# Kernel optimization log

Measured on AMD Instinct MI355X. Metric: run time of the kernel, lower is better.

## Reference

```python
import jax, jax.numpy as jnp
import numpy as np
from itertools import combinations

H_RANK_MAX = 2
TP_RANK_MAX = 2
BASIS_RANK_MAX = 2
DIM = 3
N_NODES = 50000
N_EDGES = 400000
N_CHANNELS = 16
R_CUT = 10.0  # radial cutoff for Bessel RBF (assumed)


def find_combinations(a_max, b_max, s):
    if s > a_max + b_max or s < 0:
        return []
    return [(a, s - a) for a in range(max(0, s - b_max), min(a_max, s) + 1)]


def contraction_is_valid(n_in, n_out):
    # legs are removed in pairs (Kronecker-delta contractions)
    return (n_in >= n_out) and ((n_in - n_out) % 2 == 0)


def _matchings(legs):
    # all perfect matchings of an even-size list of leg indices
    if not legs:
        yield []
        return
    a = legs[0]
    for i in range(1, len(legs)):
        rest = legs[1:i] + legs[i + 1:]
        for m in _matchings(rest):
            yield [(a, legs[i])] + m


def contraction_specs(a, b, c_out):
    # all einsum strings contracting an [E,K,dim^a] x [E,K,dim^b] tensor product
    # (a+b legs total) down to c_out free Cartesian legs, pairing the rest.
    n = a + b
    specs = []
    for free in combinations(range(n), c_out):
        paired = [i for i in range(n) if i not in free]
        for m in _matchings(paired):
            lbl = {}
            it = iter('mnopqrstuvwxyz')
            for f in free:
                lbl[f] = next(it)
            for (i, j) in m:
                L = next(it)
                lbl[i] = L
                lbl[j] = L
            sa = ''.join(lbl[i] for i in range(a))
            sb = ''.join(lbl[i] for i in range(a, n))
            so = ''.join(lbl[f] for f in free)
            specs.append(f'ek{sa},ek{sb}->ek{so}')
    return specs


def e_rbf(r, n):
    # Bessel radial basis: n is [K,1], r is [E] -> [K,E]
    return jnp.sqrt(2.0 / R_CUT) * jnp.sin(n * jnp.pi * r / R_CUT) / r


def tensor_prod(r, order):
    # repeated outer product of unit vectors: order 0 -> [E], order k -> [E] + [DIM]*k
    out = jnp.ones(r.shape[0], dtype=r.dtype)
    for _ in range(order):
        out = jnp.einsum('e...,ed->e...d', out, r)
    return out


def setup_inputs() -> dict:
    key = jax.random.key(0)
    ks = jax.random.split(key, 7)
    h0 = jax.random.normal(ks[0], (N_NODES, N_CHANNELS), jnp.float32)
    h1 = jax.random.normal(ks[1], (N_NODES, N_CHANNELS, DIM), jnp.float32)
    h2 = jax.random.normal(ks[2], (N_NODES, N_CHANNELS, DIM, DIM), jnp.float32)
    pos = jax.random.normal(ks[3], (N_NODES, DIM), jnp.float32)
    channel_weights = jax.random.normal(ks[4], (H_RANK_MAX + 1, N_CHANNELS, N_CHANNELS), jnp.float32)
    src = jax.random.randint(ks[5], (N_EDGES,), 0, N_NODES, dtype=jnp.int32)
    off = jax.random.randint(ks[6], (N_EDGES,), 1, N_NODES, dtype=jnp.int32)
    dst = (src + off) % N_NODES  # no self-loops -> no zero distances
    edge_index = jnp.stack([src, dst])
    return {"h0": h0, "h1": h1, "h2": h2, "pos": pos,
            "channel_weights": channel_weights, "edge_index": edge_index}


def reference(h0, h1, h2, pos, channel_weights, edge_index):
    h = [h0, h1, h2]
    src, dst = edge_index[0], edge_index[1]
    rel = pos[src] - pos[dst]                       # [E,3]
    dists = jnp.linalg.norm(rel, axis=-1)           # [E]
    unit = rel / dists[:, None]
    hg = [g[dst] for g in h]                        # per-edge gathered features
    # NOTE: the original forward computes channel-mixed self.h with channel_weights
    # but the contraction loop uses the UNMIXED gathered h (h[split[0]]); replicated here,
    # so channel_weights does not affect the output (zero gradient).
    n_vals = jnp.arange(1, N_CHANNELS + 1, dtype=dists.dtype)[:, None]  # [K,1]
    radial = e_rbf(dists, n_vals).reshape(N_EDGES, N_CHANNELS)  # faithful reshape (not transpose), as in source
    r_raw = [tensor_prod(unit, o) for o in range(TP_RANK_MAX + 1)]
    r_w = [jnp.einsum('ek,e...->ek...', radial, t) for t in r_raw]  # [E,K]+[3]*b
    outs = [None] * (BASIS_RANK_MAX + 1)
    for n_ind in range(H_RANK_MAX + TP_RANK_MAX + 1):
        for (a, b) in find_combinations(H_RANK_MAX, TP_RANK_MAX, n_ind):
            for br in range(BASIS_RANK_MAX + 1):
                if contraction_is_valid(n_ind, br):
                    for spec in contraction_specs(a, b, br):
                        t = jnp.einsum(spec, hg[a], r_w[b])
                        outs[br] = t if outs[br] is None else outs[br] + t
    # sum over paths (done incrementally above == stack + 'i...->...'), scatter to nodes
    res = []
    for t in outs:
        if t is not None:
            res.append(jax.ops.segment_sum(t, src, num_segments=N_NODES))
    return tuple(res)
```

## Files before the change

kernel.cpp:

```cpp
#include <hip/hip_runtime.h>
#include <math.h>

#define N_NODES   50000
#define N_EDGES   400000
#define NCH       16
#define CAP       48
#define NSTRIPE   8
#define TPB       256
#define NBN       ((N_NODES + TPB - 1) / TPB)
#define NB_EDGES  ((N_EDGES + TPB - 1) / TPB)


__global__ void build_kernel(const float* __restrict__ pos,
                             const int* __restrict__ src,
                             const int* __restrict__ dst,
                             float* __restrict__ dists,
                             int* __restrict__ cnt,
                             float4* __restrict__ edata,
                             int* __restrict__ eArr) {
    int e = blockIdx.x * TPB + threadIdx.x;
    if (e >= N_EDGES) return;
    int s = src[e];
    int d = dst[e];
    float rx = pos[3 * s + 0] - pos[3 * d + 0];
    float ry = pos[3 * s + 1] - pos[3 * d + 1];
    float rz = pos[3 * s + 2] - pos[3 * d + 2];
    float dist = sqrtf(rx * rx + ry * ry + rz * rz);
    dists[e] = dist;
    float inv = 1.0f / dist;
    int slot = atomicAdd(&cnt[s], 1);
    if (slot < CAP) {
        int idx = s * CAP + slot;
        float4 ed;
        ed.x = rx * inv;
        ed.y = ry * inv;
        ed.z = rz * inv;
        ed.w = __int_as_float(d);
        edata[idx] = ed;
        eArr[idx] = e;
    }
}

__global__ void node_wave_fast(const float* __restrict__ h0,
                               const float* __restrict__ h1,
                               const float* __restrict__ h2,
                               const int* __restrict__ cnt,
                               const float4* __restrict__ edata,
                               const int* __restrict__ eArr,
                               const float* __restrict__ dists,
                               float* __restrict__ out0,
                               float* __restrict__ out1,
                               float* __restrict__ out2) {
    int gid = blockIdx.x * TPB + threadIdx.x;
    int node = gid >> 6;
    if (node >= N_NODES) return;
    int lane = threadIdx.x & 63;
    int k = lane & 15;
    int j = lane >> 4;
    int m = cnt[node];
    if (m > CAP) m = CAP;
    int base = node * CAP;

    float acc0 = 0.0f;
    float acc1[3] = {0.0f, 0.0f, 0.0f};
    float acc2[9] = {0.0f, 0.0f, 0.0f, 0.0f, 0.0f, 0.0f, 0.0f, 0.0f, 0.0f};

    int c = j;
    float4 ed;
    int e = 0;
    if (c < m) { ed = edata[base + c]; e = eArr[base + c]; }
    while (c < m) {
        int cn = c + 4;
        float4 edn = ed;
        int en = e;
        if (cn < m) { edn = edata[base + cn]; en = eArr[base + cn]; }

        int d = __float_as_int(ed.w);

        unsigned f = (unsigned)e * NCH + (unsigned)k;
        unsigned n_idx = f / (unsigned)N_EDGES;
        unsigned e_idx = f - n_idx * (unsigned)N_EDGES;
        float r = dists[e_idx];
        float R = 0.44721359549995794f *
                  __sinf((float)(n_idx + 1) * 0.3141592653589793f * r) / r;

        float ux = ed.x, uy = ed.y, uz = ed.z;
        float u[3] = {ux, uy, uz};

        float A0 = h0[d * NCH + k];
        const float* a1p = h1 + ((size_t)d * NCH + k) * 3;
        float A1[3] = {a1p[0], a1p[1], a1p[2]};
        const float* a2p = h2 + ((size_t)d * NCH + k) * 9;
        float A2[9];
#pragma unroll
        for (int q2 = 0; q2 < 9; ++q2) A2[q2] = a2p[q2];

        float d1 = A1[0] * ux + A1[1] * uy + A1[2] * uz;
        float tA = A2[0] + A2[4] + A2[8];
        float v0 = A2[0] * ux + A2[1] * uy + A2[2] * uz;
        float v1 = A2[3] * ux + A2[4] * uy + A2[5] * uz;
        float v2 = A2[6] * ux + A2[7] * uy + A2[8] * uz;
        float w0 = A2[0] * ux + A2[3] * uy + A2[6] * uz;
        float w1 = A2[1] * ux + A2[4] * uy + A2[7] * uz;
        float w2 = A2[2] * ux + A2[5] * uy + A2[8] * uz;
        float q = ux * v0 + uy * v1 + uz * v2;

        acc0 += R * (2.0f * A0 + d1 + 2.0f * tA + 2.0f * q);

        float svw[3] = {v0 + w0, v1 + w1, v2 + w2};
        float a0t = A0 + tA;
#pragma unroll
        for (int mm = 0; mm < 3; ++mm) {
            acc1[mm] += R * (A0 * u[mm] + 2.0f * A1[mm] + 2.0f * d1 * u[mm]
                             + svw[mm] + tA * u[mm]);
#pragma unroll
            for (int nn = 0; nn < 3; ++nn) {
                acc2[3 * mm + nn] += R * (a0t * u[mm] * u[nn] + A1[mm] * u[nn]
                                          + 2.0f * A2[3 * mm + nn]
                                          + 2.0f * svw[mm] * u[nn]);
            }
        }

        ed = edn;
        e = en;
        c = cn;
    }

    acc0 += __shfl_xor(acc0, 16, 64);
    acc0 += __shfl_xor(acc0, 32, 64);
#pragma unroll
    for (int mm = 0; mm < 3; ++mm) {
        acc1[mm] += __shfl_xor(acc1[mm], 16, 64);
        acc1[mm] += __shfl_xor(acc1[mm], 32, 64);
    }
#pragma unroll
    for (int mm = 0; mm < 9; ++mm) {
        acc2[mm] += __shfl_xor(acc2[mm], 16, 64);
        acc2[mm] += __shfl_xor(acc2[mm], 32, 64);
    }

    if (j == 0) {
        int t = node * NCH + k;
        out0[t] = acc0;
        float* o1p = out1 + (size_t)t * 3;
#pragma unroll
        for (int mm = 0; mm < 3; ++mm) o1p[mm] = acc1[mm];
        float* o2p = out2 + (size_t)t * 9;
#pragma unroll
        for (int mm = 0; mm < 9; ++mm) o2p[mm] = acc2[mm];
    }
}


__global__ void fb_geom_hist(const float* __restrict__ pos,
                             const int* __restrict__ src,
                             const int* __restrict__ dst,
                             float* __restrict__ dists,
                             int* __restrict__ cnt8,
                             int* __restrict__ rankArr) {
    int e = blockIdx.x * TPB + threadIdx.x;
    if (e >= N_EDGES) return;
    int stripe = blockIdx.x & (NSTRIPE - 1);
    int s = src[e];
    int d = dst[e];
    float rx = pos[3 * s + 0] - pos[3 * d + 0];
    float ry = pos[3 * s + 1] - pos[3 * d + 1];
    float rz = pos[3 * s + 2] - pos[3 * d + 2];
    dists[e] = sqrtf(rx * rx + ry * ry + rz * rz);
    rankArr[e] = atomicAdd(&cnt8[stripe * N_NODES + s], 1);
}

__global__ void fb_scan(const int* __restrict__ cnt8,
                        int* __restrict__ incl,
                        int* __restrict__ bsum) {
    __shared__ int sh[TPB];
    int tid = threadIdx.x;
    int i = blockIdx.x * TPB + tid;
    int tot = 0;
    if (i < N_NODES) {
#pragma unroll
        for (int c = 0; c < NSTRIPE; ++c) tot += cnt8[c * N_NODES + i];
    }
    sh[tid] = tot;
    __syncthreads();
    for (int s = 1; s < TPB; s <<= 1) {
        int x = 0;
        if (tid >= s) x = sh[tid - s];
        __syncthreads();
        if (tid >= s) sh[tid] += x;
        __syncthreads();
    }
    if (i < N_NODES) incl[i] = sh[tid];
    if (tid == TPB - 1) bsum[blockIdx.x] = sh[TPB - 1];
}

__global__ void fb_final(const int* __restrict__ cnt8,
                         const int* __restrict__ incl,
                         const int* __restrict__ bsum,
                         int* __restrict__ offsets,
                         int* __restrict__ copyBase) {
    __shared__ int sh[TPB];
    int tid = threadIdx.x;
    int b = blockIdx.x;
    sh[tid] = (tid < b) ? bsum[tid] : 0;
    __syncthreads();
    for (int s = 128; s > 0; s >>= 1) {
        if (tid < s) sh[tid] += sh[tid + s];
        __syncthreads();
    }
    int base = sh[0];
    int i = b * TPB + tid;
    if (i < N_NODES) {
        int cv[NSTRIPE];
        int tot = 0;
#pragma unroll
        for (int c = 0; c < NSTRIPE; ++c) { cv[c] = cnt8[c * N_NODES + i]; tot += cv[c]; }
        int off = base + incl[i] - tot;
        offsets[i] = off;
        int run = off;
#pragma unroll
        for (int c = 0; c < NSTRIPE; ++c) { copyBase[c * N_NODES + i] = run; run += cv[c]; }
    }
    if (b == 0 && tid == 0) offsets[N_NODES] = N_EDGES;
}

__global__ void fb_fill(const int* __restrict__ src,
                        const int* __restrict__ dst,
                        const float* __restrict__ pos,
                        const float* __restrict__ dists,
                        const int* __restrict__ copyBase,
                        const int* __restrict__ rankArr,
                        float4* __restrict__ edata,
                        int* __restrict__ csr) {
    int e = blockIdx.x * TPB + threadIdx.x;
    if (e >= N_EDGES) return;
    int stripe = blockIdx.x & (NSTRIPE - 1);
    int s = src[e];
    int d = dst[e];
    float rx = pos[3 * s + 0] - pos[3 * d + 0];
    float ry = pos[3 * s + 1] - pos[3 * d + 1];
    float rz = pos[3 * s + 2] - pos[3 * d + 2];
    float inv = 1.0f / dists[e];
    int slot = copyBase[stripe * N_NODES + s] + rankArr[e];
    float4 ed;
    ed.x = rx * inv;
    ed.y = ry * inv;
    ed.z = rz * inv;
    ed.w = __int_as_float(d);
    edata[slot] = ed;
    csr[slot] = e;
}

__global__ void fb_main(const float* __restrict__ h0,
                        const float* __restrict__ h1,
                        const float* __restrict__ h2,
                        const int* __restrict__ offsets,
                        const float4* __restrict__ edata,
                        const int* __restrict__ csr,
                        const float* __restrict__ dists,
                        float* __restrict__ out0,
                        float* __restrict__ out1,
                        float* __restrict__ out2) {
    int gid = blockIdx.x * TPB + threadIdx.x;
    int node = gid >> 6;
    if (node >= N_NODES) return;
    int lane = threadIdx.x & 63;
    int k = lane & 15;
    int j = lane >> 4;
    int beg = offsets[node];
    int end = offsets[node + 1];

    float acc0 = 0.0f;
    float acc1[3] = {0.0f, 0.0f, 0.0f};
    float acc2[9] = {0.0f, 0.0f, 0.0f, 0.0f, 0.0f, 0.0f, 0.0f, 0.0f, 0.0f};

    int i = beg + j;
    float4 ed;
    int e = 0;
    if (i < end) { ed = edata[i]; e = csr[i]; }
    while (i < end) {
        int inext = i + 4;
        float4 edn = ed;
        int en = e;
        if (inext < end) { edn = edata[inext]; en = csr[inext]; }

        int d = __float_as_int(ed.w);
        unsigned f = (unsigned)e * NCH + (unsigned)k;
        unsigned n_idx = f / (unsigned)N_EDGES;
        unsigned e_idx = f - n_idx * (unsigned)N_EDGES;
        float r = dists[e_idx];
        float R = 0.44721359549995794f *
                  __sinf((float)(n_idx + 1) * 0.3141592653589793f * r) / r;

        float ux = ed.x, uy = ed.y, uz = ed.z;
        float u[3] = {ux, uy, uz};

        float A0 = h0[d * NCH + k];
        const float* a1p = h1 + ((size_t)d * NCH + k) * 3;
        float A1[3] = {a1p[0], a1p[1], a1p[2]};
        const float* a2p = h2 + ((size_t)d * NCH + k) * 9;
        float A2[9];
#pragma unroll
        for (int q2 = 0; q2 < 9; ++q2) A2[q2] = a2p[q2];

        float d1 = A1[0] * ux + A1[1] * uy + A1[2] * uz;
        float tA = A2[0] + A2[4] + A2[8];
        float v0 = A2[0] * ux + A2[1] * uy + A2[2] * uz;
        float v1 = A2[3] * ux + A2[4] * uy + A2[5] * uz;
        float v2 = A2[6] * ux + A2[7] * uy + A2[8] * uz;
        float w0 = A2[0] * ux + A2[3] * uy + A2[6] * uz;
        float w1 = A2[1] * ux + A2[4] * uy + A2[7] * uz;
        float w2 = A2[2] * ux + A2[5] * uy + A2[8] * uz;
        float q = ux * v0 + uy * v1 + uz * v2;

        acc0 += R * (2.0f * A0 + d1 + 2.0f * tA + 2.0f * q);

        float svw[3] = {v0 + w0, v1 + w1, v2 + w2};
        float a0t = A0 + tA;
#pragma unroll
        for (int mm = 0; mm < 3; ++mm) {
            acc1[mm] += R * (A0 * u[mm] + 2.0f * A1[mm] + 2.0f * d1 * u[mm]
                             + svw[mm] + tA * u[mm]);
#pragma unroll
            for (int nn = 0; nn < 3; ++nn) {
                acc2[3 * mm + nn] += R * (a0t * u[mm] * u[nn] + A1[mm] * u[nn]
                                          + 2.0f * A2[3 * mm + nn]
                                          + 2.0f * svw[mm] * u[nn]);
            }
        }

        ed = edn;
        e = en;
        i = inext;
    }

    acc0 += __shfl_xor(acc0, 16, 64);
    acc0 += __shfl_xor(acc0, 32, 64);
#pragma unroll
    for (int mm = 0; mm < 3; ++mm) {
        acc1[mm] += __shfl_xor(acc1[mm], 16, 64);
        acc1[mm] += __shfl_xor(acc1[mm], 32, 64);
    }
#pragma unroll
    for (int mm = 0; mm < 9; ++mm) {
        acc2[mm] += __shfl_xor(acc2[mm], 16, 64);
        acc2[mm] += __shfl_xor(acc2[mm], 32, 64);
    }

    if (j == 0) {
        int t = node * NCH + k;
        out0[t] = acc0;
        float* o1p = out1 + (size_t)t * 3;
#pragma unroll
        for (int mm = 0; mm < 3; ++mm) o1p[mm] = acc1[mm];
        float* o2p = out2 + (size_t)t * 9;
#pragma unroll
        for (int mm = 0; mm < 9; ++mm) o2p[mm] = acc2[mm];
    }
}


extern "C" void kernel_launch(void* const* d_in, const int* in_sizes, int n_in,
                              void* d_out, int out_size, void* d_ws, size_t ws_size,
                              hipStream_t stream) {
    const float* h0  = (const float*)d_in[0];
    const float* h1  = (const float*)d_in[1];
    const float* h2  = (const float*)d_in[2];
    const float* pos = (const float*)d_in[3];
    const int* edge_index = (const int*)d_in[5];
    const int* src = edge_index;
    const int* dst = edge_index + N_EDGES;

    float* out = (float*)d_out;
    float* out0 = out;
    float* out1 = out + (size_t)N_NODES * NCH;
    float* out2 = out + (size_t)N_NODES * NCH * 4;

    size_t need = (size_t)N_NODES * CAP * 16 + (size_t)N_NODES * CAP * 4
                + (size_t)N_EDGES * 4 + (size_t)N_NODES * 4;

    if (ws_size >= need) {
        float4* edata = (float4*)d_ws;
        int* eArr     = (int*)(edata + (size_t)N_NODES * CAP);
        float* dists  = (float*)(eArr + (size_t)N_NODES * CAP);
        int* cnt      = (int*)(dists + N_EDGES);

        hipMemsetAsync(cnt, 0, N_NODES * sizeof(int), stream);
        build_kernel<<<NB_EDGES, TPB, 0, stream>>>(pos, src, dst, dists, cnt, edata, eArr);
        node_wave_fast<<<(N_NODES * 64 + TPB - 1) / TPB, TPB, 0, stream>>>(
            h0, h1, h2, cnt, edata, eArr, dists, out0, out1, out2);
    } else {
        float4* edata   = (float4*)d_ws;
        float*  dists   = (float*)(edata + N_EDGES);
        int* cnt8       = (int*)(dists + N_EDGES);
        int* rankArr    = cnt8 + NSTRIPE * N_NODES;
        int* incl       = rankArr + N_EDGES;
        int* bsum       = incl + N_NODES;
        int* offsets    = bsum + 256;
        int* copyBase   = offsets + N_NODES + 1;
        int* csr        = copyBase + NSTRIPE * N_NODES;

        hipMemsetAsync(cnt8, 0, NSTRIPE * N_NODES * sizeof(int), stream);
        fb_geom_hist<<<NB_EDGES, TPB, 0, stream>>>(pos, src, dst, dists, cnt8, rankArr);
        fb_scan<<<NBN, TPB, 0, stream>>>(cnt8, incl, bsum);
        fb_final<<<NBN, TPB, 0, stream>>>(cnt8, incl, bsum, offsets, copyBase);
        fb_fill<<<NB_EDGES, TPB, 0, stream>>>(src, dst, pos, dists, copyBase, rankArr, edata, csr);
        fb_main<<<(N_NODES * 64 + TPB - 1) / TPB, TPB, 0, stream>>>(
            h0, h1, h2, offsets, edata, csr, dists, out0, out1, out2);
    }
}
```

Measured before the change: 182.2 us.

## Use persistent grid-stride waves and process two edges per iteration for memory-level parallelism

Rewrites the main node kernel as a persistent grid-stride loop over nodes with a fixed block count. Each lane now gathers the h0/h1/h2 sets and distances for two edges before doing the math, which puts more memory requests in flight. It also sets launch bounds for occupancy and writes outputs with nontemporal stores. The extra live registers from holding two gathered edge sets could reduce occupancy. The first two edata loads happen unconditionally, so they may read unused slots before the count check.

Result: slower. 453.0 us (+148.7%).

```diff
diff --git a/kernel.cpp b/kernel.cpp
--- a/kernel.cpp
+++ b/kernel.cpp
@@ -9,6 +9,7 @@
 #define TPB       256
 #define NBN       ((N_NODES + TPB - 1) / TPB)
 #define NB_EDGES  ((N_EDGES + TPB - 1) / TPB)
+#define NBLK_MAIN 4096
 
 
 __global__ void build_kernel(const float* __restrict__ pos,
@@ -41,113 +42,160 @@
     }
 }
 
-__global__ void node_wave_fast(const float* __restrict__ h0,
-                               const float* __restrict__ h1,
-                               const float* __restrict__ h2,
-                               const int* __restrict__ cnt,
-                               const float4* __restrict__ edata,
-                               const int* __restrict__ eArr,
-                               const float* __restrict__ dists,
-                               float* __restrict__ out0,
-                               float* __restrict__ out1,
-                               float* __restrict__ out2) {
-    int gid = blockIdx.x * TPB + threadIdx.x;
-    int node = gid >> 6;
-    if (node >= N_NODES) return;
+__device__ __forceinline__ void edge_math(
+    float ux, float uy, float uz, float R,
+    float A0, const float A1[3], const float A2[9],
+    float& acc0, float acc1[3], float acc2[9])
+{
+    float u[3] = {ux, uy, uz};
+    float d1 = A1[0] * ux + A1[1] * uy + A1[2] * uz;
+    float tA = A2[0] + A2[4] + A2[8];
+    float v0 = A2[0] * ux + A2[1] * uy + A2[2] * uz;
+    float v1 = A2[3] * ux + A2[4] * uy + A2[5] * uz;
+    float v2 = A2[6] * ux + A2[7] * uy + A2[8] * uz;
+    float w0 = A2[0] * ux + A2[3] * uy + A2[6] * uz;
+    float w1 = A2[1] * ux + A2[4] * uy + A2[7] * uz;
+    float w2 = A2[2] * ux + A2[5] * uy + A2[8] * uz;
+    float q = ux * v0 + uy * v1 + uz * v2;
+
+    acc0 += R * (2.0f * A0 + d1 + 2.0f * tA + 2.0f * q);
+
+    float svw[3] = {v0 + w0, v1 + w1, v2 + w2};
+    float a0t = A0 + tA;
+#pragma unroll
+    for (int mm = 0; mm < 3; ++mm) {
+        acc1[mm] += R * (A0 * u[mm] + 2.0f * A1[mm] + 2.0f * d1 * u[mm]
+                         + svw[mm] + tA * u[mm]);
+#pragma unroll
+        for (int nn = 0; nn < 3; ++nn) {
+            acc2[3 * mm + nn] += R * (a0t * u[mm] * u[nn] + A1[mm] * u[nn]
+                                      + 2.0f * A2[3 * mm + nn]
+                                      + 2.0f * svw[mm] * u[nn]);
+        }
+    }
+}
+
+__device__ __forceinline__ void load_hset(
+    const float* __restrict__ h0, const float* __restrict__ h1,
+    const float* __restrict__ h2, const float* __restrict__ dists,
+    int d, int e, int k,
+    float& A0, float A1[3], float A2[9], float& r, float& nf)
+{
+    A0 = h0[d * NCH + k];
+    const float* p1 = h1 + ((size_t)d * NCH + k) * 3;
+    A1[0] = p1[0]; A1[1] = p1[1]; A1[2] = p1[2];
+    const float* p2 = h2 + ((size_t)d * NCH + k) * 9;
+#pragma unroll
+    for (int q2 = 0; q2 < 9; ++q2) A2[q2] = p2[q2];
+    unsigned f = (unsigned)e * NCH + (unsigned)k;
+    unsigned n_idx = f / (unsigned)N_EDGES;
+    unsigned e_idx = f - n_idx * (unsigned)N_EDGES;
+    r = dists[e_idx];
+    nf = (float)(n_idx + 1);
+}
+
+__device__ __forceinline__ float radial_R(float nf, float r) {
+    return 0.44721359549995794f * __sinf(nf * 0.3141592653589793f * r) / r;
+}
+
+__global__ __launch_bounds__(TPB, 6)
+void node_wave_fast(const float* __restrict__ h0,
+                    const float* __restrict__ h1,
+                    const float* __restrict__ h2,
+                    const int* __restrict__ cnt,
+                    const float4* __restrict__ edata,
+                    const int* __restrict__ eArr,
+                    const float* __restrict__ dists,
+                    float* __restrict__ out0,
+                    float* __restrict__ out1,
+                    float* __restrict__ out2) {
     int lane = threadIdx.x & 63;
     int k = lane & 15;
     int j = lane >> 4;
-    int m = cnt[node];
-    if (m > CAP) m = CAP;
-    int base = node * CAP;
-
-    float acc0 = 0.0f;
-    float acc1[3] = {0.0f, 0.0f, 0.0f};
-    float acc2[9] = {0.0f, 0.0f, 0.0f, 0.0f, 0.0f, 0.0f, 0.0f, 0.0f, 0.0f};
-
-    int c = j;
-    float4 ed;
-    int e = 0;
-    if (c < m) { ed = edata[base + c]; e = eArr[base + c]; }
-    while (c < m) {
-        int cn = c + 4;
-        float4 edn = ed;
-        int en = e;
-        if (cn < m) { edn = edata[base + cn]; en = eArr[base + cn]; }
-
-        int d = __float_as_int(ed.w);
-
-        unsigned f = (unsigned)e * NCH + (unsigned)k;
-        unsigned n_idx = f / (unsigned)N_EDGES;
-        unsigned e_idx = f - n_idx * (unsigned)N_EDGES;
-        float r = dists[e_idx];
-        float R = 0.44721359549995794f *
-                  __sinf((float)(n_idx + 1) * 0.3141592653589793f * r) / r;
-
-        float ux = ed.x, uy = ed.y, uz = ed.z;
-        float u[3] = {ux, uy, uz};
-
-        float A0 = h0[d * NCH + k];
-        const float* a1p = h1 + ((size_t)d * NCH + k) * 3;
-        float A1[3] = {a1p[0], a1p[1], a1p[2]};
-        const float* a2p = h2 + ((size_t)d * NCH + k) * 9;
-        float A2[9];
-#pragma unroll
-        for (int q2 = 0; q2 < 9; ++q2) A2[q2] = a2p[q2];
-
-        float d1 = A1[0] * ux + A1[1] * uy + A1[2] * uz;
-        float tA = A2[0] + A2[4] + A2[8];
-        float v0 = A2[0] * ux + A2[1] * uy + A2[2] * uz;
-        float v1 = A2[3] * ux + A2[4] * uy + A2[5] * uz;
-        float v2 = A2[6] * ux + A2[7] * uy + A2[8] * uz;
-        float w0 = A2[0] * ux + A2[3] * uy + A2[6] * uz;
-        float w1 = A2[1] * ux + A2[4] * uy + A2[7] * uz;
-        float w2 = A2[2] * ux + A2[5] * uy + A2[8] * uz;
-        float q = ux * v0 + uy * v1 + uz * v2;
-
-        acc0 += R * (2.0f * A0 + d1 + 2.0f * tA + 2.0f * q);
-
-        float svw[3] = {v0 + w0, v1 + w1, v2 + w2};
-        float a0t = A0 + tA;
+    int wid = blockIdx.x * (TPB >> 6) + (threadIdx.x >> 6);
+    const int nw = NBLK_MAIN * (TPB >> 6);
+
+    for (int node = wid; node < N_NODES; node += nw) {
+        int base = node * CAP;
+        int m = cnt[node];
+        float4 edA = edata[base + j];
+        float4 edB = edata[base + j + 4];
+        int eA = eArr[base + j];
+        int eB = eArr[base + j + 4];
+        if (m > CAP) m = CAP;
+
+        float acc0 = 0.0f;
+        float acc1[3] = {0.0f, 0.0f, 0.0f};
+        float acc2[9] = {0.0f, 0.0f, 0.0f, 0.0f, 0.0f, 0.0f, 0.0f, 0.0f, 0.0f};
+
+        bool hasA = (j < m);
+        bool hasB = (j + 4 < m);
+
+        float A0A, A1A[3], A2A[9], rA, nfA;
+        float A0B, A1B[3], A2B[9], rB, nfB;
+        if (hasA) load_hset(h0, h1, h2, dists, __float_as_int(edA.w), eA, k,
+                            A0A, A1A, A2A, rA, nfA);
+        if (hasB) load_hset(h0, h1, h2, dists, __float_as_int(edB.w), eB, k,
+                            A0B, A1B, A2B, rB, nfB);
+        if (hasA) {
+            float R = radial_R(nfA, rA);
+            edge_math(edA.x, edA.y, edA.z, R, A0A, A1A, A2A, acc0, acc1, acc2);
+        }
+        if (hasB) {
+            float R = radial_R(nfB, rB);
+            edge_math(edB.x, edB.y, edB.z, R, A0B, A1B, A2B, acc0, acc1, acc2);
+        }
+
+        for (int c = j + 8; c < m; c += 8) {
+            float4 eda = edata[base + c];
+            int ea = eArr[base + c];
+            bool hb = (c + 4) < m;
+            float4 edb;
+            int eb = 0;
+            if (hb) { edb = edata[base + c + 4]; eb = eArr[base + c + 4]; }
+
+            float a0a, a1a[3], a2a[9], ra, nfa;
+            load_hset(h0, h1, h2, dists, __float_as_int(eda.w), ea, k,
+                      a0a, a1a, a2a, ra, nfa);
+            float a0b, a1b[3], a2b[9], rb, nfb;
+            if (hb) load_hset(h0, h1, h2, dists, __float_as_int(edb.w), eb, k,
+                              a0b, a1b, a2b, rb, nfb);
+
+            {
+                float R = radial_R(nfa, ra);
+                edge_math(eda.x, eda.y, eda.z, R, a0a, a1a, a2a, acc0, acc1, acc2);
+            }
+            if (hb) {
+                float R = radial_R(nfb, rb);
+                edge_math(edb.x, edb.y, edb.z, R, a0b, a1b, a2b, acc0, acc1, acc2);
+            }
+        }
+
+        acc0 += __shfl_xor(acc0, 16, 64);
+        acc0 += __shfl_xor(acc0, 32, 64);
 #pragma unroll
         for (int mm = 0; mm < 3; ++mm) {
-            acc1[mm] += R * (A0 * u[mm] + 2.0f * A1[mm] + 2.0f * d1 * u[mm]
-                             + svw[mm] + tA * u[mm]);
-#pragma unroll
-            for (int nn = 0; nn < 3; ++nn) {
-                acc2[3 * mm + nn] += R * (a0t * u[mm] * u[nn] + A1[mm] * u[nn]
-                                          + 2.0f * A2[3 * mm + nn]
-                                          + 2.0f * svw[mm] * u[nn]);
-            }
-        }
-
-        ed = edn;
-        e = en;
-        c = cn;
-    }
-
-    acc0 += __shfl_xor(acc0, 16, 64);
-    acc0 += __shfl_xor(acc0, 32, 64);
-#pragma unroll
-    for (int mm = 0; mm < 3; ++mm) {
-        acc1[mm] += __shfl_xor(acc1[mm], 16, 64);
-        acc1[mm] += __shfl_xor(acc1[mm], 32, 64);
-    }
-#pragma unroll
-    for (int mm = 0; mm < 9; ++mm) {
-        acc2[mm] += __shfl_xor(acc2[mm], 16, 64);
-        acc2[mm] += __shfl_xor(acc2[mm], 32, 64);
-    }
-
-    if (j == 0) {
-        int t = node * NCH + k;
-        out0[t] = acc0;
-        float* o1p = out1 + (size_t)t * 3;
-#pragma unroll
-        for (int mm = 0; mm < 3; ++mm) o1p[mm] = acc1[mm];
-        float* o2p = out2 + (size_t)t * 9;
-#pragma unroll
-        for (int mm = 0; mm < 9; ++mm) o2p[mm] = acc2[mm];
+            acc1[mm] += __shfl_xor(acc1[mm], 16, 64);
+            acc1[mm] += __shfl_xor(acc1[mm], 32, 64);
+        }
+#pragma unroll
+        for (int mm = 0; mm < 9; ++mm) {
+            acc2[mm] += __shfl_xor(acc2[mm], 16, 64);
+            acc2[mm] += __shfl_xor(acc2[mm], 32, 64);
+        }
+
+        if (j == 0) {
+            int t = node * NCH + k;
+            __builtin_nontemporal_store(acc0, &out0[t]);
+            float* o1p = out1 + (size_t)t * 3;
+#pragma unroll
+            for (int mm = 0; mm < 3; ++mm)
+                __builtin_nontemporal_store(acc1[mm], o1p + mm);
+            float* o2p = out2 + (size_t)t * 9;
+#pragma unroll
+            for (int mm = 0; mm < 9; ++mm)
+                __builtin_nontemporal_store(acc2[mm], o2p + mm);
+        }
     }
 }
 
@@ -285,49 +333,10 @@
         if (inext < end) { edn = edata[inext]; en = csr[inext]; }
 
         int d = __float_as_int(ed.w);
-        unsigned f = (unsigned)e * NCH + (unsigned)k;
-        unsigned n_idx = f / (unsigned)N_EDGES;
-        unsigned e_idx = f - n_idx * (unsigned)N_EDGES;
-        float r = dists[e_idx];
-        float R = 0.44721359549995794f *
-                  __sinf((float)(n_idx + 1) * 0.3141592653589793f * r) / r;
-
-        float ux = ed.x, uy = ed.y, uz = ed.z;
-        float u[3] = {ux, uy, uz};
-
-        float A0 = h0[d * NCH + k];
-        const float* a1p = h1 + ((size_t)d * NCH + k) * 3;
-        float A1[3] = {a1p[0], a1p[1], a1p[2]};
-        const float* a2p = h2 + ((size_t)d * NCH + k) * 9;
-        float A2[9];
-#pragma unroll
-        for (int q2 = 0; q2 < 9; ++q2) A2[q2] = a2p[q2];
-
-        float d1 = A1[0] * ux + A1[1] * uy + A1[2] * uz;
-        float tA = A2[0] + A2[4] + A2[8];
-        float v0 = A2[0] * ux + A2[1] * uy + A2[2] * uz;
-        float v1 = A2[3] * ux + A2[4] * uy + A2[5] * uz;
-        float v2 = A2[6] * ux + A2[7] * uy + A2[8] * uz;
-        float w0 = A2[0] * ux + A2[3] * uy + A2[6] * uz;
-        float w1 = A2[1] * ux + A2[4] * uy + A2[7] * uz;
-        float w2 = A2[2] * ux + A2[5] * uy + A2[8] * uz;
-        float q = ux * v0 + uy * v1 + uz * v2;
-
-        acc0 += R * (2.0f * A0 + d1 + 2.0f * tA + 2.0f * q);
-
-        float svw[3] = {v0 + w0, v1 + w1, v2 + w2};
-        float a0t = A0 + tA;
-#pragma unroll
-        for (int mm = 0; mm < 3; ++mm) {
-            acc1[mm] += R * (A0 * u[mm] + 2.0f * A1[mm] + 2.0f * d1 * u[mm]
-                             + svw[mm] + tA * u[mm]);
-#pragma unroll
-            for (int nn = 0; nn < 3; ++nn) {
-                acc2[3 * mm + nn] += R * (a0t * u[mm] * u[nn] + A1[mm] * u[nn]
-                                          + 2.0f * A2[3 * mm + nn]
-                                          + 2.0f * svw[mm] * u[nn]);
-            }
-        }
+        float a0, a1[3], a2[9], r, nf;
+        load_hset(h0, h1, h2, dists, d, e, k, a0, a1, a2, r, nf);
+        float R = radial_R(nf, r);
+        edge_math(ed.x, ed.y, ed.z, R, a0, a1, a2, acc0, acc1, acc2);
 
         ed = edn;
         e = en;
@@ -387,7 +396,7 @@
 
         hipMemsetAsync(cnt, 0, N_NODES * sizeof(int), stream);
         build_kernel<<<NB_EDGES, TPB, 0, stream>>>(pos, src, dst, dists, cnt, edata, eArr);
-        node_wave_fast<<<(N_NODES * 64 + TPB - 1) / TPB, TPB, 0, stream>>>(
+        node_wave_fast<<<NBLK_MAIN, TPB, 0, stream>>>(
             h0, h1, h2, cnt, edata, eArr, dists, out0, out1, out2);
     } else {
         float4* edata   = (float4*)d_ws;
```
